# Kernel optimization log

Measured on AMD Instinct MI355X. Metric: run time of the kernel, lower is better.

## Reference

```python
import jax, jax.numpy as jnp
import numpy as np


def setup_inputs() -> dict:
    key = jax.random.key(0)
    ks = jax.random.split(key, 5)
    B, S, D = 4, 2048, 1024
    x = jax.random.normal(ks[0], (B, S, D), dtype=jnp.float32)
    wq = jax.random.normal(ks[1], (D, D), dtype=jnp.float32) * (D ** -0.5)
    wk = jax.random.normal(ks[2], (D, D), dtype=jnp.float32) * (D ** -0.5)
    wv = jax.random.normal(ks[3], (D, D), dtype=jnp.float32) * (D ** -0.5)
    wo = jax.random.normal(ks[4], (D, D), dtype=jnp.float32) * (D ** -0.5)
    return {"x": x, "wq": wq, "wk": wk, "wv": wv, "wo": wo, "n_heads": 16}


def reference(x, wq, wk, wv, wo, n_heads):
    B, S, D = x.shape
    hd = D // n_heads
    # projections (module computes x @ w.T)
    q = (x @ wq.T).reshape(B, S, n_heads, hd).transpose(0, 2, 1, 3)  # b h s d
    k = (x @ wk.T).reshape(B, S, n_heads, hd).transpose(0, 2, 1, 3)
    v = (x @ wv.T).reshape(B, S, n_heads, hd).transpose(0, 2, 1, 3)
    # NOTE: module scales by sqrt(d_model), not sqrt(head_dim)
    scores = jnp.einsum("bhqd,bhkd->bhqk", q, k) / jnp.sqrt(jnp.float32(D))
    # module bug preserved: masked_fill(mask == 0, -1e9) with mask = triu(diag=1)
    # fills positions where mask is False (lower triangle incl. diagonal).
    triu_mask = jnp.triu(jnp.ones((S, S), dtype=bool), k=1)  # True strictly above diag
    scores = jnp.where(triu_mask, scores, jnp.float32(-1e9))
    attn = jax.nn.softmax(scores, axis=-1)
    out = jnp.einsum("bhqk,bhkd->bhqd", attn, v)  # b h s d
    out = out.transpose(0, 2, 1, 3).reshape(B, S, D)
    return out @ wo.T
```

## Files before the change

### kernel.cpp

```cpp
#include <hip/hip_runtime.h>
#include <hip/hip_bf16.h>

typedef __attribute__((ext_vector_type(8))) short short8;
typedef __attribute__((ext_vector_type(4))) short bfx4;
typedef __attribute__((ext_vector_type(4))) float floatx4;
typedef __attribute__((ext_vector_type(4))) __fp16 h4_t;
typedef __attribute__((ext_vector_type(2))) __fp16 h2_t;
typedef __attribute__((ext_vector_type(8))) __fp16 h8_t;

#define BATCH 4
#define SEQ 2048
#define D_MODEL 1024
#define NH 16
#define HD 64
#define ELEMS 8388608
#define WELEMS 1048576

__device__ __forceinline__ unsigned short f2bf(float f) {
    union { float f; unsigned u; } x; x.f = f;
    unsigned r = x.u + 0x7FFFu + ((x.u >> 16) & 1u);
    return (unsigned short)(r >> 16);
}
__device__ __forceinline__ unsigned short f2h(float f) {
    union { __fp16 h; unsigned short u; } x;
    x.h = (__fp16)f;
    return x.u;
}

#if __has_builtin(__builtin_amdgcn_exp2f)
__device__ __forceinline__ float fexp2(float x) { return __builtin_amdgcn_exp2f(x); }
#else
__device__ __forceinline__ float fexp2(float x) { return exp2f(x); }
#endif

__device__ __forceinline__ void gll16(const void* g, const void* l) {
    __builtin_amdgcn_global_load_lds(
        (const __attribute__((address_space(1))) void*)g,
        (__attribute__((address_space(3))) void*)l,
        16, 0, 0);
}


__global__ __launch_bounds__(256)
void cvt_kernel(const float* __restrict__ x,  const float* __restrict__ wq,
                const float* __restrict__ wk, const float* __restrict__ wv,
                const float* __restrict__ wo,
                unsigned short* __restrict__ xbf,
                unsigned short* __restrict__ wqkv,
                unsigned short* __restrict__ wobf)
{
    size_t idx = ((size_t)blockIdx.x * 256 + threadIdx.x) * 8;
    const float* src; unsigned short* dst; size_t off;
    if (idx < (size_t)ELEMS)                    { src = x;  dst = xbf;             off = idx; }
    else if (idx < (size_t)ELEMS + WELEMS)      { src = wq; dst = wqkv;            off = idx - ELEMS; }
    else if (idx < (size_t)ELEMS + 2 * WELEMS)  { src = wk; dst = wqkv + WELEMS;   off = idx - ELEMS - WELEMS; }
    else if (idx < (size_t)ELEMS + 3 * WELEMS)  { src = wv; dst = wqkv + 2*WELEMS; off = idx - ELEMS - 2*WELEMS; }
    else                                        { src = wo; dst = wobf;            off = idx - ELEMS - 3*WELEMS; }
    floatx4 a = *(const floatx4*)(src + off);
    floatx4 b = *(const floatx4*)(src + off + 4);
    short8 v;
#pragma unroll
    for (int d = 0; d < 4; d++) { v[d] = (short)f2bf(a[d]); v[4+d] = (short)f2bf(b[d]); }
    *(short8*)(dst + off) = v;
}

__global__ __launch_bounds__(256, 2)
void gemm_qkv3_kernel(const unsigned short* __restrict__ A,
                      const unsigned short* __restrict__ B,
                      unsigned short* __restrict__ Qb,
                      unsigned short* __restrict__ Kb,
                      unsigned short* __restrict__ Vb)
{
    __shared__ __align__(16) unsigned short As[128 * 64];
    __shared__ __align__(16) unsigned short Bs[128 * 64];

    const int t = threadIdx.x;
    const int wave = t >> 6, lane = t & 63;
    const int lm = lane & 15, lq = lane >> 4;
    const int wrow = (wave >> 1) * 64, wcol = (wave & 1) * 64;
    const int m0 = blockIdx.x * 128, n0 = blockIdx.y * 128;
    const int lrow = lane >> 3, lg = lane & 7;
    const int gsw = lg ^ lrow;

    floatx4 acc[4][4] = {};

    for (int k0 = 0; k0 < 1024; k0 += 64) {
        __syncthreads();
#pragma unroll
        for (int i = 0; i < 4; i++) {
            int rows8 = wave * 32 + i * 8;
            gll16(A + (size_t)(m0 + rows8 + lrow) * 1024 + k0 + gsw * 8, As + rows8 * 64);
            gll16(B + (size_t)(n0 + rows8 + lrow) * 1024 + k0 + gsw * 8, Bs + rows8 * 64);
        }
        __syncthreads();

#pragma unroll
        for (int c = 0; c < 2; c++) {
            short8 af[4], bfr[4];
#pragma unroll
            for (int i = 0; i < 4; i++) {
                int ra = wrow + i * 16 + lm;
                int g = c * 4 + lq;
                af[i] = *(const short8*)(As + (ra * 8 + (g ^ (ra & 7))) * 8);
            }
#pragma unroll
            for (int j = 0; j < 4; j++) {
                int rb = wcol + j * 16 + lm;
                int g = c * 4 + lq;
                bfr[j] = *(const short8*)(Bs + (rb * 8 + (g ^ (rb & 7))) * 8);
            }
#pragma unroll
            for (int i = 0; i < 4; i++)
#pragma unroll
                for (int j = 0; j < 4; j++)
                    acc[i][j] = __builtin_amdgcn_mfma_f32_16x16x32_bf16(
                        af[i], bfr[j], acc[i][j], 0, 0, 0);
        }
    }

    const int z = n0 >> 10;
#pragma unroll
    for (int i = 0; i < 4; i++)
#pragma unroll
        for (int j = 0; j < 4; j++)
#pragma unroll
            for (int r = 0; r < 4; r++) {
                int gm = m0 + wrow + i * 16 + lq * 4 + r;
                int gn = n0 + wcol + j * 16 + lm;
                int nl = gn & 1023, h = nl >> 6, d = nl & 63;
                int b = gm >> 11, s = gm & 2047;
                float v = acc[i][j][r];
                size_t bh = (size_t)(b * NH + h);
                if (z == 0)      Qb[(bh * SEQ + s) * HD + d] = f2bf(v);
                else if (z == 1) Kb[(bh * SEQ + s) * HD + d] = f2bf(v);
                else             Vb[(bh * HD + d) * SEQ + s] = f2h(v);
            }
}

__global__ __launch_bounds__(256, 2)
void gemm_out3_kernel(const unsigned short* __restrict__ A,
                      const unsigned short* __restrict__ B,
                      float* __restrict__ Out)
{
    __shared__ __align__(16) unsigned short As[128 * 64];
    __shared__ __align__(16) unsigned short Bs[128 * 64];

    const int t = threadIdx.x;
    const int wave = t >> 6, lane = t & 63;
    const int lm = lane & 15, lq = lane >> 4;
    const int wrow = (wave >> 1) * 64, wcol = (wave & 1) * 64;
    const int m0 = blockIdx.x * 128, n0 = blockIdx.y * 128;
    const int lrow = lane >> 3, lg = lane & 7;
    const int gsw = lg ^ lrow;

    floatx4 acc[4][4] = {};

    for (int k0 = 0; k0 < 1024; k0 += 64) {
        __syncthreads();
#pragma unroll
        for (int i = 0; i < 4; i++) {
            int rows8 = wave * 32 + i * 8;
            gll16(A + (size_t)(m0 + rows8 + lrow) * 1024 + k0 + gsw * 8, As + rows8 * 64);
            gll16(B + (size_t)(n0 + rows8 + lrow) * 1024 + k0 + gsw * 8, Bs + rows8 * 64);
        }
        __syncthreads();

#pragma unroll
        for (int c = 0; c < 2; c++) {
            short8 af[4], bfr[4];
#pragma unroll
            for (int i = 0; i < 4; i++) {
                int ra = wrow + i * 16 + lm;
                int g = c * 4 + lq;
                af[i] = *(const short8*)(As + (ra * 8 + (g ^ (ra & 7))) * 8);
            }
#pragma unroll
            for (int j = 0; j < 4; j++) {
                int rb = wcol + j * 16 + lm;
                int g = c * 4 + lq;
                bfr[j] = *(const short8*)(Bs + (rb * 8 + (g ^ (rb & 7))) * 8);
            }
#pragma unroll
            for (int i = 0; i < 4; i++)
#pragma unroll
                for (int j = 0; j < 4; j++)
                    acc[i][j] = __builtin_amdgcn_mfma_f32_16x16x32_bf16(
                        af[i], bfr[j], acc[i][j], 0, 0, 0);
        }
    }

#pragma unroll
    for (int i = 0; i < 4; i++)
#pragma unroll
        for (int j = 0; j < 4; j++)
#pragma unroll
            for (int r = 0; r < 4; r++) {
                int gm = m0 + wrow + i * 16 + lq * 4 + r;
                int gn = n0 + wcol + j * 16 + lm;
                Out[(size_t)gm * D_MODEL + gn] = acc[i][j][r];
            }
}

#define PROCESS_SUB(KSB, VSB, KT, DOMASK)                                      \
    do {                                                                       \
        _Pragma("unroll")                                                      \
        for (int jt = 0; jt < 8; jt++) {                                       \
            floatx4 sc0 = {}, sc1 = {};                                        \
            _Pragma("unroll")                                                  \
            for (int c = 0; c < 2; c++) {                                      \
                int row_ = jt * 16 + lm;                                       \
                int g_ = c * 4 + lq;                                           \
                short8 kf = *(const short8*)((KSB) + (row_ * 8 + (g_ ^ (row_ & 7))) * 8); \
                sc0 = __builtin_amdgcn_mfma_f32_16x16x32_bf16(kf, bq0[c], sc0, 0, 0, 0); \
                sc1 = __builtin_amdgcn_mfma_f32_16x16x32_bf16(kf, bq1[c], sc1, 0, 0, 0); \
            }                                                                  \
            if (DOMASK) {                                                      \
                _Pragma("unroll")                                              \
                for (int r = 0; r < 4; r++) {                                  \
                    int kj = (KT) * 128 + jt * 16 + lq * 4 + r;                \
                    if (!(kj > q0)) sc0[r] = -3.2e10f;                         \
                    if (!(kj > q1)) sc1[r] = -3.2e10f;                         \
                }                                                              \
            }                                                                  \
            float p00 = fexp2(sc0[0] * kA), p01 = fexp2(sc0[1] * kA);          \
            float p02 = fexp2(sc0[2] * kA), p03 = fexp2(sc0[3] * kA);          \
            float p10 = fexp2(sc1[0] * kA), p11 = fexp2(sc1[1] * kA);          \
            float p12 = fexp2(sc1[2] * kA), p13 = fexp2(sc1[3] * kA);          \
            l0 += (p00 + p01) + (p02 + p03);                                   \
            l1 += (p10 + p11) + (p12 + p13);                                   \
            h2_t a0_ = __builtin_amdgcn_cvt_pkrtz(p00, p01);                   \
            h2_t b0_ = __builtin_amdgcn_cvt_pkrtz(p02, p03);                   \
            h2_t a1_ = __builtin_amdgcn_cvt_pkrtz(p10, p11);                   \
            h2_t b1_ = __builtin_amdgcn_cvt_pkrtz(p12, p13);                   \
            h4_t pf0, pf1;                                                     \
            pf0[0] = a0_[0]; pf0[1] = a0_[1]; pf0[2] = b0_[0]; pf0[3] = b0_[1];\
            pf1[0] = a1_[0]; pf1[1] = a1_[1]; pf1[2] = b1_[0]; pf1[3] = b1_[1];\
            _Pragma("unroll")                                                  \
            for (int jd = 0; jd < 4; jd++) {                                   \
                int rowv_ = jd * 16 + lm;                                      \
                int g16_ = jt * 2 + (lq >> 1);                                 \
                int slot_ = rowv_ * 16 + (g16_ ^ lm);                          \
                h4_t vf = *(const h4_t*)((VSB) + slot_ * 8 + (lq & 1) * 4);    \
                acc0[jd] = __builtin_amdgcn_mfma_f32_16x16x16f16(vf, pf0, acc0[jd], 0, 0, 0); \
                acc1[jd] = __builtin_amdgcn_mfma_f32_16x16x16f16(vf, pf1, acc1[jd], 0, 0, 0); \
            }                                                                  \
        }                                                                      \
    } while (0)

#define WRITE_O(QROW, ACC, LV)                                                 \
    do {                                                                       \
        float l_ = LV;                                                         \
        l_ += __shfl_xor(l_, 16); l_ += __shfl_xor(l_, 32);                    \
        float inv_ = 1.0f / l_;                                                \
        _Pragma("unroll")                                                      \
        for (int jd = 0; jd < 4; jd++) {                                       \
            bfx4 o_;                                                           \
            _Pragma("unroll")                                                  \
            for (int r = 0; r < 4; r++) o_[r] = (short)f2bf(ACC[jd][r] * inv_);\
            *(bfx4*)(O + (size_t)(b * SEQ + (QROW)) * D_MODEL + h * HD + jd * 16 + lq * 4) = o_; \
        }                                                                      \
    } while (0)

__global__ __launch_bounds__(256, 2)
void attn10_kernel(const unsigned short* __restrict__ Q,
                   const unsigned short* __restrict__ K,
                   const unsigned short* __restrict__ V,
                   unsigned short* __restrict__ O)
{
    __shared__ __align__(16) unsigned short Ks[2 * 128 * 64];
    __shared__ __align__(16) unsigned short Vs[2 * 64 * 128];

    const int t = threadIdx.x;
    const int wave = t >> 6, lane = t & 63;
    const int lm = lane & 15, lq = lane >> 4;

    const int orig = blockIdx.x;
    const int wkid = (orig & 7) * 128 + (orig >> 3);
    const int bh = wkid >> 4;
    const int j  = wkid & 15;

    const int q0 = j * 128 + wave * 16 + lm;
    const int q1 = q0 + 64;

    const unsigned short* Qh = Q + (size_t)bh * SEQ * HD;
    const unsigned short* Kh = K + (size_t)bh * SEQ * HD;
    const unsigned short* Vh = V + (size_t)bh * HD * SEQ;

    short8 bq0[2], bq1[2];
#pragma unroll
    for (int c = 0; c < 2; c++) {
        bq0[c] = *(const short8*)(Qh + (size_t)q0 * HD + c * 32 + lq * 8);
        bq1[c] = *(const short8*)(Qh + (size_t)q1 * HD + c * 32 + lq * 8);
    }

    floatx4 acc0[4] = {}, acc1[4] = {};
    float l0 = 0.f, l1 = 0.f;
    const float kA = 0.04508422002778011f;

    const int lrow = lane >> 3, lg = lane & 7;
    const int tmin = j >> 1;

    for (int tt = 7; tt >= tmin; tt--) {
        __syncthreads();
#pragma unroll
        for (int h2 = 0; h2 < 2; h2++) {
#pragma unroll
            for (int i = 0; i < 4; i++) {
                int rows8 = wave * 32 + i * 8;
                gll16(Kh + (size_t)(tt * 256 + h2 * 128 + rows8 + lrow) * HD + (lg ^ lrow) * 8,
                      Ks + h2 * (128 * 64) + rows8 * 64);
            }
#pragma unroll
            for (int i = 0; i < 4; i++) {
                int rows4 = wave * 16 + i * 4;
                int row = rows4 + (lane >> 4);
                int g = (lane & 15) ^ (row & 15);
                gll16(Vh + (size_t)row * SEQ + tt * 256 + h2 * 128 + g * 8,
                      Vs + h2 * (64 * 128) + rows4 * 128);
            }
        }
        __syncthreads();

        const int s_lo = (tt == tmin && (j & 1)) ? 1 : 0;
#pragma unroll 1
        for (int s = 1; s >= s_lo; s--) {
            const unsigned short* Ksb = Ks + s * (128 * 64);
            const __fp16* Vsb = (const __fp16*)(Vs + s * (64 * 128));
            const bool domask = (tt == tmin) && (s == (j & 1));
            const int kt = tt * 2 + s;
            PROCESS_SUB(Ksb, Vsb, kt, domask);
        }
    }

    const int b = bh >> 4, h = bh & 15;
    WRITE_O(q0, acc0, l0);
    WRITE_O(q1, acc1, l1);
}

__global__ __launch_bounds__(256, 2)
void row2047_kernel(const unsigned short* __restrict__ V,
                    unsigned short* __restrict__ O)
{
    __shared__ float red[256];
    const int bh = blockIdx.x;
    const int b = bh >> 4, h = bh & 15;
    const int t = threadIdx.x;
    const int d = t & 63, seg = t >> 6;
    const __fp16* Vh = (const __fp16*)V + (size_t)bh * HD * SEQ + (size_t)d * SEQ + seg * 512;
    float s = 0.f;
    for (int i = 0; i < 512; i += 8) {
        h8_t v = *(const h8_t*)(Vh + i);
#pragma unroll
        for (int j = 0; j < 8; j++) s += (float)v[j];
    }
    red[t] = s;
    __syncthreads();
    if (seg == 0) {
        float tot = red[d] + red[64 + d] + red[128 + d] + red[192 + d];
        O[(size_t)(b * SEQ + 2047) * D_MODEL + h * HD + d] = f2bf(tot * (1.f / 2048.f));
    }
}

__global__ __launch_bounds__(256, 2)
void gemm_qkv_kernel(const float* __restrict__ A,
                     const float* __restrict__ W0,
                     const float* __restrict__ W1,
                     const float* __restrict__ W2,
                     unsigned short* __restrict__ O0,
                     unsigned short* __restrict__ O1,
                     unsigned short* __restrict__ O2)
{
    const int K = 1024;
    const float* W;
    unsigned short* Out;
    if (blockIdx.z == 0)      { W = W0; Out = O0; }
    else if (blockIdx.z == 1) { W = W1; Out = O1; }
    else                      { W = W2; Out = O2; }

    __shared__ __align__(16) unsigned short As[128 * 64];
    __shared__ __align__(16) unsigned short Bs[128 * 64];

    const int t = threadIdx.x;
    const int wave = t >> 6, lane = t & 63;
    const int lm = lane & 15, lq = lane >> 4;
    const int wrow = (wave >> 1) * 64, wcol = (wave & 1) * 64;
    const int m0 = blockIdx.x * 128, n0 = blockIdx.y * 128;

    floatx4 acc[4][4] = {};

    for (int k0 = 0; k0 < K; k0 += 64) {
        __syncthreads();
#pragma unroll
        for (int rr = 0; rr < 4; rr++) {
            int p = rr * 256 + t;
            int row = p >> 3, g = p & 7;
            const float* pa = A + (size_t)(m0 + row) * K + k0 + g * 8;
            const float* pw = W + (size_t)(n0 + row) * K + k0 + g * 8;
            floatx4 a0 = *(const floatx4*)pa, a1 = *(const floatx4*)(pa + 4);
            floatx4 w0 = *(const floatx4*)pw, w1 = *(const floatx4*)(pw + 4);
            short8 va, vb;
#pragma unroll
            for (int d = 0; d < 4; d++) {
                va[d]     = (short)f2bf(a0[d]);
                va[4 + d] = (short)f2bf(a1[d]);
                vb[d]     = (short)f2bf(w0[d]);
                vb[4 + d] = (short)f2bf(w1[d]);
            }
            int dst = row * 8 + (g ^ (row & 7));
            *(short8*)(As + dst * 8) = va;
            *(short8*)(Bs + dst * 8) = vb;
        }
        __syncthreads();

        short8 af[4][2], bf[4][2];
#pragma unroll
        for (int i = 0; i < 4; i++)
#pragma unroll
            for (int c = 0; c < 2; c++) {
                int ra = wrow + i * 16 + lm;
                int rb = wcol + i * 16 + lm;
                int g = c * 4 + lq;
                af[i][c] = *(const short8*)(As + (ra * 8 + (g ^ (ra & 7))) * 8);
                bf[i][c] = *(const short8*)(Bs + (rb * 8 + (g ^ (rb & 7))) * 8);
            }
#pragma unroll
        for (int i = 0; i < 4; i++)
#pragma unroll
            for (int j = 0; j < 4; j++)
#pragma unroll
                for (int c = 0; c < 2; c++)
                    acc[i][j] = __builtin_amdgcn_mfma_f32_16x16x32_bf16(
                        af[i][c], bf[j][c], acc[i][j], 0, 0, 0);
    }

    const int zi = blockIdx.z;
#pragma unroll
    for (int i = 0; i < 4; i++)
#pragma unroll
        for (int j = 0; j < 4; j++)
#pragma unroll
            for (int r = 0; r < 4; r++) {
                int gm = m0 + wrow + i * 16 + lq * 4 + r;
                int gn = n0 + wcol + j * 16 + lm;
                int b = gm >> 11, s = gm & 2047;
                int h = gn >> 6, d = gn & 63;
                if (zi == 2) {
                    Out[((size_t)(b * NH + h) * HD + d) * SEQ + s] = f2h(acc[i][j][r]);
                } else {
                    Out[((size_t)(b * NH + h) * SEQ + s) * HD + d] = f2bf(acc[i][j][r]);
                }
            }
}

__global__ __launch_bounds__(256, 2)
void gemm_out_kernel(const unsigned short* __restrict__ Abf,
                     const float* __restrict__ W,
                     float* __restrict__ Out)
{
    const int K = 1024;
    __shared__ __align__(16) unsigned short As[128 * 64];
    __shared__ __align__(16) unsigned short Bs[128 * 64];

    const int t = threadIdx.x;
    const int wave = t >> 6, lane = t & 63;
    const int lm = lane & 15, lq = lane >> 4;
    const int wrow = (wave >> 1) * 64, wcol = (wave & 1) * 64;
    const int m0 = blockIdx.x * 128, n0 = blockIdx.y * 128;

    floatx4 acc[4][4] = {};

    for (int k0 = 0; k0 < K; k0 += 64) {
        __syncthreads();
#pragma unroll
        for (int rr = 0; rr < 4; rr++) {
            int p = rr * 256 + t;
            int row = p >> 3, g = p & 7;
            short8 va = *(const short8*)(Abf + (size_t)(m0 + row) * K + k0 + g * 8);
            const float* pw = W + (size_t)(n0 + row) * K + k0 + g * 8;
            floatx4 w0 = *(const floatx4*)pw, w1 = *(const floatx4*)(pw + 4);
            short8 vb;
#pragma unroll
            for (int d = 0; d < 4; d++) {
                vb[d]     = (short)f2bf(w0[d]);
                vb[4 + d] = (short)f2bf(w1[d]);
            }
            int dst = row * 8 + (g ^ (row & 7));
            *(short8*)(As + dst * 8) = va;
            *(short8*)(Bs + dst * 8) = vb;
        }
        __syncthreads();

        short8 af[4][2], bf[4][2];
#pragma unroll
        for (int i = 0; i < 4; i++)
#pragma unroll
            for (int c = 0; c < 2; c++) {
                int ra = wrow + i * 16 + lm;
                int rb = wcol + i * 16 + lm;
                int g = c * 4 + lq;
                af[i][c] = *(const short8*)(As + (ra * 8 + (g ^ (ra & 7))) * 8);
                bf[i][c] = *(const short8*)(Bs + (rb * 8 + (g ^ (rb & 7))) * 8);
            }
#pragma unroll
        for (int i = 0; i < 4; i++)
#pragma unroll
            for (int j = 0; j < 4; j++)
#pragma unroll
                for (int c = 0; c < 2; c++)
                    acc[i][j] = __builtin_amdgcn_mfma_f32_16x16x32_bf16(
                        af[i][c], bf[j][c], acc[i][j], 0, 0, 0);
    }

#pragma unroll
    for (int i = 0; i < 4; i++)
#pragma unroll
        for (int j = 0; j < 4; j++)
#pragma unroll
            for (int r = 0; r < 4; r++) {
                int gm = m0 + wrow + i * 16 + lq * 4 + r;
                int gn = n0 + wcol + j * 16 + lm;
                Out[(size_t)gm * D_MODEL + gn] = acc[i][j][r];
            }
}

extern "C" void kernel_launch(void* const* d_in, const int* in_sizes, int n_in,
                              void* d_out, int out_size, void* d_ws, size_t ws_size,
                              hipStream_t stream) {
    const float* x  = (const float*)d_in[0];
    const float* wq = (const float*)d_in[1];
    const float* wk = (const float*)d_in[2];
    const float* wv = (const float*)d_in[3];
    const float* wo = (const float*)d_in[4];

    unsigned short* ws = (unsigned short*)d_ws;
    const bool fast = ws_size >= (size_t)36 * 1024 * 1024 * 2;

    if (fast) {
        unsigned short* xbf  = ws;
        unsigned short* wqkv = ws + (size_t)ELEMS;
        unsigned short* wobf = ws + (size_t)ELEMS + 3 * WELEMS;
        unsigned short* Qb   = ws + (size_t)ELEMS + 4 * WELEMS;
        unsigned short* Kb   = Qb + ELEMS;
        unsigned short* Vb   = Kb + ELEMS;
        unsigned short* Ob   = xbf;

        cvt_kernel<<<6144, 256, 0, stream>>>(x, wq, wk, wv, wo, xbf, wqkv, wobf);
        gemm_qkv3_kernel<<<dim3(64, 24), 256, 0, stream>>>(xbf, wqkv, Qb, Kb, Vb);
        attn10_kernel<<<1024, 256, 0, stream>>>(Qb, Kb, Vb, Ob);
        row2047_kernel<<<BATCH * NH, 256, 0, stream>>>(Vb, Ob);
        gemm_out3_kernel<<<dim3(64, 8), 256, 0, stream>>>(Ob, wobf, (float*)d_out);
    } else {
        unsigned short* Qb = ws;
        unsigned short* Kb = Qb + ELEMS;
        unsigned short* Vb = Kb + ELEMS;
        unsigned short* Ob = Vb + ELEMS;

        gemm_qkv_kernel<<<dim3(64, 8, 3), 256, 0, stream>>>(x, wq, wk, wv, Qb, Kb, Vb);
        attn10_kernel<<<1024, 256, 0, stream>>>(Qb, Kb, Vb, Ob);
        row2047_kernel<<<BATCH * NH, 256, 0, stream>>>(Vb, Ob);
        gemm_out_kernel<<<dim3(64, 8), 256, 0, stream>>>(Ob, wo, (float*)d_out);
    }
}
```

Measured before the change: 272.1 us.

## Double-buffer K/V tiles in attention to overlap loads with compute

Replaces the load-all-then-compute loop over 256-key chunks with a ping-pong pipeline over 128-key tiles. The next K/V tile is issued into the alternate LDS buffer with async global-to-LDS loads while the current tile is processed, and a vmcnt wait plus barrier sits between steps. This is meant to hide global load latency behind the MFMA work. LDS use stays the same; the cost is more barriers and finer-grained steps.

```diff
diff --git a/kernel.cpp b/kernel.cpp
--- a/kernel.cpp
+++ b/kernel.cpp
@@ -200,6 +200,24 @@
                 Out[(size_t)gm * D_MODEL + gn] = acc[i][j][r];
             }
 }
+
+#define STAGE_KV(KS, VS, KT)                                                   \
+    do {                                                                       \
+        _Pragma("unroll")                                                      \
+        for (int i_ = 0; i_ < 4; i_++) {                                       \
+            int rows8_ = wave * 32 + i_ * 8;                                   \
+            gll16(Kh + (size_t)((KT) * 128 + rows8_ + lrow) * HD + (lg ^ lrow) * 8, \
+                  (KS) + rows8_ * 64);                                         \
+        }                                                                      \
+        _Pragma("unroll")                                                      \
+        for (int i_ = 0; i_ < 4; i_++) {                                       \
+            int rows4_ = wave * 16 + i_ * 4;                                   \
+            int row_ = rows4_ + (lane >> 4);                                   \
+            int g_ = (lane & 15) ^ (row_ & 15);                                \
+            gll16(Vh + (size_t)row_ * SEQ + (KT) * 128 + g_ * 8,               \
+                  (VS) + rows4_ * 128);                                        \
+        }                                                                      \
+    } while (0)
 
 #define PROCESS_SUB(KSB, VSB, KT, DOMASK)                                      \
     do {                                                                       \
@@ -261,14 +279,23 @@
         }                                                                      \
     } while (0)
 
+#define DRAIN_BAR()                                                            \
+    do {                                                                       \
+        asm volatile("s_waitcnt vmcnt(0)" ::: "memory");                       \
+        __builtin_amdgcn_s_barrier();                                          \
+        __builtin_amdgcn_sched_barrier(0);                                     \
+    } while (0)
+
 __global__ __launch_bounds__(256, 2)
-void attn10_kernel(const unsigned short* __restrict__ Q,
+void attn11_kernel(const unsigned short* __restrict__ Q,
                    const unsigned short* __restrict__ K,
                    const unsigned short* __restrict__ V,
                    unsigned short* __restrict__ O)
 {
-    __shared__ __align__(16) unsigned short Ks[2 * 128 * 64];
-    __shared__ __align__(16) unsigned short Vs[2 * 64 * 128];
+    __shared__ __align__(16) unsigned short KsA[128 * 64];
+    __shared__ __align__(16) unsigned short VsA[64 * 128];
+    __shared__ __align__(16) unsigned short KsB[128 * 64];
+    __shared__ __align__(16) unsigned short VsB[64 * 128];
 
     const int t = threadIdx.x;
     const int wave = t >> 6, lane = t & 63;
@@ -298,38 +325,22 @@
     const float kA = 0.04508422002778011f;
 
     const int lrow = lane >> 3, lg = lane & 7;
-    const int tmin = j >> 1;
-
-    for (int tt = 7; tt >= tmin; tt--) {
-        __syncthreads();
-#pragma unroll
-        for (int h2 = 0; h2 < 2; h2++) {
-#pragma unroll
-            for (int i = 0; i < 4; i++) {
-                int rows8 = wave * 32 + i * 8;
-                gll16(Kh + (size_t)(tt * 256 + h2 * 128 + rows8 + lrow) * HD + (lg ^ lrow) * 8,
-                      Ks + h2 * (128 * 64) + rows8 * 64);
-            }
-#pragma unroll
-            for (int i = 0; i < 4; i++) {
-                int rows4 = wave * 16 + i * 4;
-                int row = rows4 + (lane >> 4);
-                int g = (lane & 15) ^ (row & 15);
-                gll16(Vh + (size_t)row * SEQ + tt * 256 + h2 * 128 + g * 8,
-                      Vs + h2 * (64 * 128) + rows4 * 128);
-            }
-        }
-        __syncthreads();
-
-        const int s_lo = (tt == tmin && (j & 1)) ? 1 : 0;
-#pragma unroll 1
-        for (int s = 1; s >= s_lo; s--) {
-            const unsigned short* Ksb = Ks + s * (128 * 64);
-            const __fp16* Vsb = (const __fp16*)(Vs + s * (64 * 128));
-            const bool domask = (tt == tmin) && (s == (j & 1));
-            const int kt = tt * 2 + s;
-            PROCESS_SUB(Ksb, Vsb, kt, domask);
-        }
+
+    STAGE_KV(KsA, VsA, 15);
+    DRAIN_BAR();
+
+    int kt = 15;
+    while (true) {
+        if (kt - 1 >= j) STAGE_KV(KsB, VsB, kt - 1);
+        PROCESS_SUB(KsA, (const __fp16*)VsA, kt, (kt == j));
+        if (kt - 1 < j) break;
+        DRAIN_BAR();
+        kt--;
+        if (kt - 1 >= j) STAGE_KV(KsA, VsA, kt - 1);
+        PROCESS_SUB(KsB, (const __fp16*)VsB, kt, (kt == j));
+        if (kt - 1 < j) break;
+        DRAIN_BAR();
+        kt--;
     }
 
     const int b = bh >> 4, h = bh & 15;
@@ -546,7 +557,7 @@
 
         cvt_kernel<<<6144, 256, 0, stream>>>(x, wq, wk, wv, wo, xbf, wqkv, wobf);
         gemm_qkv3_kernel<<<dim3(64, 24), 256, 0, stream>>>(xbf, wqkv, Qb, Kb, Vb);
-        attn10_kernel<<<1024, 256, 0, stream>>>(Qb, Kb, Vb, Ob);
+        attn11_kernel<<<1024, 256, 0, stream>>>(Qb, Kb, Vb, Ob);
         row2047_kernel<<<BATCH * NH, 256, 0, stream>>>(Vb, Ob);
         gemm_out3_kernel<<<dim3(64, 8), 256, 0, stream>>>(Ob, wobf, (float*)d_out);
     } else {
@@ -556,7 +567,7 @@
         unsigned short* Ob = Vb + ELEMS;
 
         gemm_qkv_kernel<<<dim3(64, 8, 3), 256, 0, stream>>>(x, wq, wk, wv, Qb, Kb, Vb);
-        attn10_kernel<<<1024, 256, 0, stream>>>(Qb, Kb, Vb, Ob);
+        attn11_kernel<<<1024, 256, 0, stream>>>(Qb, Kb, Vb, Ob);
         row2047_kernel<<<BATCH * NH, 256, 0, stream>>>(Vb, Ob);
         gemm_out_kernel<<<dim3(64, 8), 256, 0, stream>>>(Ob, wo, (float*)d_out);
     }
```

New measurement: 270.1 us. About the same (-0.7%).
